# Kernel optimization log

Measured on AMD Instinct MI355X. Metric: run time of the kernel, lower is better.

The kernel has to match this reference:

```python
import jax, jax.numpy as jnp
import numpy as np

BN_EPS = 1e-5
K_HOPS = 10


def setup_inputs() -> dict:
    key = jax.random.key(0)
    ks = jax.random.split(key, 8)
    N, F, H, C, E = 169343, 128, 256, 40, 1200000
    return {
        "x": jax.random.normal(ks[0], (N, F), dtype=jnp.float32),
        "edge_index": jax.random.randint(ks[1], (2, E), 0, N, dtype=jnp.int64),
        "norm": jax.random.uniform(ks[2], (E,), dtype=jnp.float32),
        "W1": jax.random.normal(ks[3], (F, H), dtype=jnp.float32) * (1.0 / np.sqrt(F)),
        "b1": jnp.zeros((H,), jnp.float32),
        "bn_gamma": jnp.ones((H,), jnp.float32),
        "bn_beta": jnp.zeros((H,), jnp.float32),
        "bn_mean": jnp.zeros((H,), jnp.float32),
        "bn_var": jnp.ones((H,), jnp.float32),
        "W2": jax.random.normal(ks[4], (H, C), dtype=jnp.float32) * (1.0 / np.sqrt(H)),
        "b2": jnp.zeros((C,), jnp.float32),
        "proj_w": jax.random.normal(ks[5], (C,), dtype=jnp.float32) * (1.0 / np.sqrt(C)),
        "proj_b": jnp.zeros((1,), jnp.float32),
    }


def reference(x, edge_index, norm, W1, b1, bn_gamma, bn_beta, bn_mean, bn_var,
              W2, b2, proj_w, proj_b):
    N = x.shape[0]
    src, dst = edge_index[0], edge_index[1]

    # MLP head: Linear -> BatchNorm (eval, running stats) -> ReLU -> Linear
    h = x @ W1 + b1
    h = (h - bn_mean) * jax.lax.rsqrt(bn_var + BN_EPS) * bn_gamma + bn_beta
    h = jax.nn.relu(h)  # dropout: identity at inference
    h = h @ W2 + b2  # [N, C]

    # K-hop norm-weighted scatter-add propagation, collecting snapshots
    def hop(carry, _):
        msgs = norm[:, None] * carry[src]              # [E, C]
        nxt = jax.ops.segment_sum(msgs, dst, num_segments=N)
        return nxt, nxt

    _, hops = jax.lax.scan(hop, h, None, length=K_HOPS)  # [K, N, C]
    pps = jnp.concatenate([h[None], hops], axis=0)       # [K+1, N, C]
    pps = jnp.transpose(pps, (1, 0, 2))                  # [N, K+1, C]

    # sigmoid attention over hops, weighted combine
    retain = jax.nn.sigmoid(pps @ proj_w + proj_b[0])    # [N, K+1]
    out = jnp.einsum("nk,nkc->nc", retain, pps)          # [N, C]
    return jax.nn.log_softmax(out, axis=1)
```

## Files before the change

### kernel.cpp

```cpp
#include <hip/hip_runtime.h>
#include <hip/hip_bf16.h>
#include <math.h>

#define F 128
#define H 256
#define C 40
#define KHOPS 10
#define TM 64
#define HK 64

__global__ void k_count(const int* __restrict__ dst, int E, int* __restrict__ cnt) {
    int e = blockIdx.x * 256 + threadIdx.x;
    if (e < E) atomicAdd(&cnt[dst[e]], 1);
}

__global__ void k_scan1(const int* __restrict__ cnt, int n, int* __restrict__ bsum) {
    __shared__ int sh[256];
    int t = threadIdx.x;
    int base = blockIdx.x * 4096 + t * 16;
    int s = 0;
    for (int i = 0; i < 16; i++) { int idx = base + i; if (idx < n) s += cnt[idx]; }
    sh[t] = s; __syncthreads();
    for (int o = 128; o > 0; o >>= 1) {
        if (t < o) sh[t] += sh[t + o];
        __syncthreads();
    }
    if (t == 0) bsum[blockIdx.x] = sh[0];
}

__global__ void k_scan2(int* __restrict__ bsum, int nb) {
    if (threadIdx.x == 0) {
        int acc = 0;
        for (int i = 0; i < nb; i++) { int v = bsum[i]; bsum[i] = acc; acc += v; }
    }
}

__global__ void k_scan3(const int* __restrict__ cnt, int n, const int* __restrict__ bsum,
                        int* __restrict__ rp) {
    __shared__ int sh[256];
    int t = threadIdx.x;
    int base = blockIdx.x * 4096 + t * 16;
    int local[16]; int s = 0;
    for (int i = 0; i < 16; i++) {
        int idx = base + i;
        int v = (idx < n) ? cnt[idx] : 0;
        local[i] = v; s += v;
    }
    sh[t] = s; __syncthreads();
    for (int o = 1; o < 256; o <<= 1) {
        int v = (t >= o) ? sh[t - o] : 0;
        __syncthreads();
        sh[t] += v;
        __syncthreads();
    }
    int excl = (t == 0) ? 0 : sh[t - 1];
    int run = bsum[blockIdx.x] + excl;
    for (int i = 0; i < 16; i++) {
        int idx = base + i;
        if (idx < n) { rp[idx] = run; run += local[i]; }
    }
}

__global__ void k_fill(const int* __restrict__ src, const int* __restrict__ dst,
                       const float* __restrict__ nrm, int E, const int* __restrict__ rp,
                       int* __restrict__ cur, int2* __restrict__ ep) {
    int e = blockIdx.x * 256 + threadIdx.x;
    if (e < E) {
        int d = dst[e];
        int p = rp[d] + atomicAdd(&cur[d], 1);
        ep[p] = make_int2(src[e], __float_as_int(nrm[e]));
    }
}

__launch_bounds__(256, 2)
__global__ void k_mlp(const float* __restrict__ x, const float* __restrict__ W1,
                      const float* __restrict__ b1, const float* __restrict__ g,
                      const float* __restrict__ be, const float* __restrict__ mu,
                      const float* __restrict__ var, const float* __restrict__ W2,
                      const float* __restrict__ b2, const float* __restrict__ pw,
                      const float* __restrict__ pb,
                      float* __restrict__ h, float* __restrict__ oacc, int N) {
    __shared__ float xs[TM][132];
    __shared__ float h1s[TM][68];
    __shared__ float w2s[C][68];
    __shared__ float asc[HK], dsc[HK];
    __shared__ float redc[256];
    __shared__ float sigv[TM];

    int t = threadIdx.x;
    int n0 = blockIdx.x * TM;

    for (int k = 0; k < 8; k++) {
        int idx = k * 256 + t;
        int node = idx >> 5, f4 = idx & 31;
        int n = n0 + node;
        float4 v = (n < N) ? ((const float4*)x)[(size_t)n * (F / 4) + f4]
                           : make_float4(0.f, 0.f, 0.f, 0.f);
        *((float4*)&xs[node][f4 * 4]) = v;
    }

    float acc2[10];
    {
        int cg = t & 3;
        #pragma unroll
        for (int j = 0; j < 10; j++) acc2[j] = b2[cg * 10 + j];
    }

    int tn = t & 15, th = t >> 4;
    const float4* W1g = (const float4*)W1;

    for (int h0 = 0; h0 < H; h0 += HK) {
        for (int k = 0; k < 10; k++) {
            int idx = k * 256 + t;
            int hh = idx / 40, c = idx % 40;
            w2s[c][hh] = W2[(size_t)(h0 + hh) * C + c];
        }
        if (t < HK) {
            int hg = h0 + t;
            float a = g[hg] * rsqrtf(var[hg] + 1e-5f);
            asc[t] = a;
            dsc[t] = (b1[hg] - mu[hg]) * a + be[hg];
        }
        __syncthreads();

        float acc[4][4];
        #pragma unroll
        for (int i = 0; i < 4; i++)
            #pragma unroll
            for (int j = 0; j < 4; j++) acc[i][j] = 0.f;

        #pragma unroll 4
        for (int f0 = 0; f0 < F; f0 += 4) {
            float4 wv[4];
            #pragma unroll
            for (int q = 0; q < 4; q++)
                wv[q] = W1g[(size_t)(f0 + q) * (H / 4) + (h0 >> 2) + th];
            float4 xv[4];
            #pragma unroll
            for (int i = 0; i < 4; i++)
                xv[i] = *((const float4*)&xs[tn + 16 * i][f0]);
            #pragma unroll
            for (int i = 0; i < 4; i++) {
                float xa[4] = {xv[i].x, xv[i].y, xv[i].z, xv[i].w};
                #pragma unroll
                for (int q = 0; q < 4; q++) {
                    float wa[4] = {wv[q].x, wv[q].y, wv[q].z, wv[q].w};
                    #pragma unroll
                    for (int j = 0; j < 4; j++) acc[i][j] += xa[q] * wa[j];
                }
            }
        }
        #pragma unroll
        for (int i = 0; i < 4; i++) {
            float4 o;
            float* po = (float*)&o;
            #pragma unroll
            for (int j = 0; j < 4; j++) {
                int hh = th * 4 + j;
                float v = acc[i][j] * asc[hh] + dsc[hh];
                po[j] = v > 0.f ? v : 0.f;
            }
            *((float4*)&h1s[tn + 16 * i][th * 4]) = o;
        }
        __syncthreads();

        int n_loc = t >> 2, cg = t & 3;
        #pragma unroll 4
        for (int hh = 0; hh < HK; hh += 4) {
            float4 hv = *((const float4*)&h1s[n_loc][hh]);
            #pragma unroll
            for (int j = 0; j < 10; j++) {
                float4 w4 = *((const float4*)&w2s[cg * 10 + j][hh]);
                acc2[j] += hv.x * w4.x + hv.y * w4.y + hv.z * w4.z + hv.w * w4.w;
            }
        }
        __syncthreads();
    }

    int n_loc = t >> 2, cg = t & 3;
    int n = n0 + n_loc;
    float part = 0.f;
    #pragma unroll
    for (int j = 0; j < 10; j++) part += acc2[j] * pw[cg * 10 + j];
    redc[t] = part;
    __syncthreads();
    if (cg == 0) {
        float s = redc[n_loc * 4] + redc[n_loc * 4 + 1] + redc[n_loc * 4 + 2] + redc[n_loc * 4 + 3];
        sigv[n_loc] = 1.f / (1.f + expf(-(s + pb[0])));
    }
    __syncthreads();
    if (n < N) {
        float sg = sigv[n_loc];
        #pragma unroll
        for (int j = 0; j < 10; j++) {
            h[(size_t)n * C + cg * 10 + j] = acc2[j];
            oacc[(size_t)n * C + cg * 10 + j] = sg * acc2[j];
        }
    }
}

__global__ void k_hop(const float4* __restrict__ cur4, float4* __restrict__ nxt4,
                      float4* __restrict__ oacc4, const int* __restrict__ rp,
                      const int2* __restrict__ ep,
                      const float* __restrict__ pw, const float* __restrict__ pb, int N) {
    __shared__ float red[320];
    __shared__ float sig[64];
    int t = threadIdx.x;
    int nl = t / 5, p = t % 5;
    int n = blockIdx.x * 64 + nl;
    int c0 = 2 * p;
    float4 a0 = make_float4(0.f, 0.f, 0.f, 0.f);
    float4 a1 = make_float4(0.f, 0.f, 0.f, 0.f);
    if (n < N) {
        int b = rp[n], e = rp[n + 1];
        int j = b;
        for (; j + 4 <= e; j += 4) {
            int2 e0 = ep[j], e1 = ep[j + 1], e2 = ep[j + 2], e3 = ep[j + 3];
            const float4* r0 = cur4 + (size_t)e0.x * 10 + c0;
            const float4* r1 = cur4 + (size_t)e1.x * 10 + c0;
            const float4* r2 = cur4 + (size_t)e2.x * 10 + c0;
            const float4* r3 = cur4 + (size_t)e3.x * 10 + c0;
            float4 v00 = r0[0], v01 = r0[1];
            float4 v10 = r1[0], v11 = r1[1];
            float4 v20 = r2[0], v21 = r2[1];
            float4 v30 = r3[0], v31 = r3[1];
            float w0 = __int_as_float(e0.y), w1 = __int_as_float(e1.y);
            float w2 = __int_as_float(e2.y), w3 = __int_as_float(e3.y);
            a0.x += w0 * v00.x; a0.y += w0 * v00.y; a0.z += w0 * v00.z; a0.w += w0 * v00.w;
            a1.x += w0 * v01.x; a1.y += w0 * v01.y; a1.z += w0 * v01.z; a1.w += w0 * v01.w;
            a0.x += w1 * v10.x; a0.y += w1 * v10.y; a0.z += w1 * v10.z; a0.w += w1 * v10.w;
            a1.x += w1 * v11.x; a1.y += w1 * v11.y; a1.z += w1 * v11.z; a1.w += w1 * v11.w;
            a0.x += w2 * v20.x; a0.y += w2 * v20.y; a0.z += w2 * v20.z; a0.w += w2 * v20.w;
            a1.x += w2 * v21.x; a1.y += w2 * v21.y; a1.z += w2 * v21.z; a1.w += w2 * v21.w;
            a0.x += w3 * v30.x; a0.y += w3 * v30.y; a0.z += w3 * v30.z; a0.w += w3 * v30.w;
            a1.x += w3 * v31.x; a1.y += w3 * v31.y; a1.z += w3 * v31.z; a1.w += w3 * v31.w;
        }
        if (j + 2 <= e) {
            int2 e0 = ep[j], e1 = ep[j + 1];
            const float4* r0 = cur4 + (size_t)e0.x * 10 + c0;
            const float4* r1 = cur4 + (size_t)e1.x * 10 + c0;
            float4 v00 = r0[0], v01 = r0[1];
            float4 v10 = r1[0], v11 = r1[1];
            float w0 = __int_as_float(e0.y), w1 = __int_as_float(e1.y);
            a0.x += w0 * v00.x; a0.y += w0 * v00.y; a0.z += w0 * v00.z; a0.w += w0 * v00.w;
            a1.x += w0 * v01.x; a1.y += w0 * v01.y; a1.z += w0 * v01.z; a1.w += w0 * v01.w;
            a0.x += w1 * v10.x; a0.y += w1 * v10.y; a0.z += w1 * v10.z; a0.w += w1 * v10.w;
            a1.x += w1 * v11.x; a1.y += w1 * v11.y; a1.z += w1 * v11.z; a1.w += w1 * v11.w;
            j += 2;
        }
        if (j < e) {
            int2 e0 = ep[j];
            const float4* r0 = cur4 + (size_t)e0.x * 10 + c0;
            float4 v00 = r0[0], v01 = r0[1];
            float w0 = __int_as_float(e0.y);
            a0.x += w0 * v00.x; a0.y += w0 * v00.y; a0.z += w0 * v00.z; a0.w += w0 * v00.w;
            a1.x += w0 * v01.x; a1.y += w0 * v01.y; a1.z += w0 * v01.z; a1.w += w0 * v01.w;
        }
        nxt4[(size_t)n * 10 + c0] = a0;
        nxt4[(size_t)n * 10 + c0 + 1] = a1;
    }
    float4 pw0 = ((const float4*)pw)[c0];
    float4 pw1 = ((const float4*)pw)[c0 + 1];
    red[t] = a0.x * pw0.x + a0.y * pw0.y + a0.z * pw0.z + a0.w * pw0.w
           + a1.x * pw1.x + a1.y * pw1.y + a1.z * pw1.z + a1.w * pw1.w;
    __syncthreads();
    if (p == 0) {
        float s = red[t] + red[t + 1] + red[t + 2] + red[t + 3] + red[t + 4];
        sig[nl] = 1.f / (1.f + expf(-(s + pb[0])));
    }
    __syncthreads();
    if (n < N) {
        float sg = sig[nl];
        size_t o = (size_t)n * 10 + c0;
        float4 v0 = oacc4[o], v1 = oacc4[o + 1];
        v0.x += sg * a0.x; v0.y += sg * a0.y; v0.z += sg * a0.z; v0.w += sg * a0.w;
        v1.x += sg * a1.x; v1.y += sg * a1.y; v1.z += sg * a1.z; v1.w += sg * a1.w;
        oacc4[o] = v0;
        oacc4[o + 1] = v1;
    }
}

__global__ void k_lsm(float4* __restrict__ io, int N) {
    __shared__ float red[320];
    __shared__ float statm[32];
    __shared__ float stats[32];
    int t = threadIdx.x;
    int nl = t / 10, c4 = t % 10;
    int n = blockIdx.x * 32 + nl;
    bool ok = n < N;
    float4 v = ok ? io[(size_t)n * 10 + c4] : make_float4(-1e30f, -1e30f, -1e30f, -1e30f);
    red[t] = fmaxf(fmaxf(v.x, v.y), fmaxf(v.z, v.w));
    __syncthreads();
    if (c4 == 0) {
        float m = -1e30f;
        #pragma unroll
        for (int q = 0; q < 10; q++) m = fmaxf(m, red[nl * 10 + q]);
        statm[nl] = m;
    }
    __syncthreads();
    float m = statm[nl];
    float e0 = expf(v.x - m), e1 = expf(v.y - m), e2 = expf(v.z - m), e3 = expf(v.w - m);
    red[t] = e0 + e1 + e2 + e3;
    __syncthreads();
    if (c4 == 0) {
        float s = 0.f;
        #pragma unroll
        for (int q = 0; q < 10; q++) s += red[nl * 10 + q];
        stats[nl] = logf(s);
    }
    __syncthreads();
    if (ok) {
        float ls = stats[nl];
        io[(size_t)n * 10 + c4] = make_float4(v.x - m - ls, v.y - m - ls, v.z - m - ls, v.w - m - ls);
    }
}

extern "C" void kernel_launch(void* const* d_in, const int* in_sizes, int n_in,
                              void* d_out, int out_size, void* d_ws, size_t ws_size,
                              hipStream_t stream) {
    const float* x   = (const float*)d_in[0];
    const int*   ei  = (const int*)d_in[1];
    const float* nrm = (const float*)d_in[2];
    const float* W1  = (const float*)d_in[3];
    const float* b1  = (const float*)d_in[4];
    const float* g   = (const float*)d_in[5];
    const float* be  = (const float*)d_in[6];
    const float* mu  = (const float*)d_in[7];
    const float* var = (const float*)d_in[8];
    const float* W2  = (const float*)d_in[9];
    const float* b2  = (const float*)d_in[10];
    const float* pw  = (const float*)d_in[11];
    const float* pb  = (const float*)d_in[12];
    float* out = (float*)d_out;

    int N = in_sizes[0] / F;
    int E = in_sizes[2];

    char* w = (char*)d_ws;
    auto alloc = [&](size_t bytes) {
        void* p = (void*)w;
        w += ((bytes + 255) / 256) * 256;
        return p;
    };
    int*   rp     = (int*)alloc((size_t)(N + 1) * 4);
    int*   cursor = (int*)alloc((size_t)(N + 1) * 4);
    int*   bsum   = (int*)alloc(256 * 4);
    int2*  ep     = (int2*)alloc((size_t)E * 8);
    float* bufA   = (float*)alloc((size_t)N * C * 4);
    float* bufB   = (float*)alloc((size_t)N * C * 4);

    hipMemsetAsync(cursor, 0, (size_t)(N + 1) * 4, stream);

    k_count<<<(E + 255) / 256, 256, 0, stream>>>(ei + E, E, cursor);

    int n1 = N + 1;
    int NB = (n1 + 4095) / 4096;
    k_scan1<<<NB, 256, 0, stream>>>(cursor, n1, bsum);
    k_scan2<<<1, 64, 0, stream>>>(bsum, NB);
    k_scan3<<<NB, 256, 0, stream>>>(cursor, n1, bsum, rp);

    hipMemsetAsync(cursor, 0, (size_t)(N + 1) * 4, stream);
    k_fill<<<(E + 255) / 256, 256, 0, stream>>>(ei, ei + E, nrm, E, rp, cursor, ep);

    k_mlp<<<(N + TM - 1) / TM, 256, 0, stream>>>(x, W1, b1, g, be, mu, var, W2, b2,
                                                 pw, pb, bufA, out, N);

    int nodeBlocks64 = (N + 63) / 64;
    float* cur = bufA;
    float* nxt = bufB;
    for (int k = 0; k < KHOPS; k++) {
        k_hop<<<nodeBlocks64, 320, 0, stream>>>((const float4*)cur, (float4*)nxt, (float4*)out,
                                                rp, ep, pw, pb, N);
        float* tmp = cur; cur = nxt; nxt = tmp;
    }

    int nodeBlocks32 = (N + 31) / 32;
    k_lsm<<<nodeBlocks32, 320, 0, stream>>>((float4*)out, N);
}
```

Measured before the change: 1.136 ms.

## Pad hop feature rows to 64 floats and read transposed W2 from global

Hop feature buffers are padded to a 64-float row pitch, chosen only when the workspace is large enough, so that each gathered node row lines up with 256-byte boundaries during the scatter-gather hops. W2 is pre-transposed by a small kernel and the MLP reads it straight from global/L2 rather than staging it in shared memory each tile. Occupancy is raised to 3 blocks per CU, and outputs are written as coalesced float4 stores through LDS. The padding adds memory footprint and bandwidth on the writes, and the uncached W2 reads may add latency.

```diff
diff --git a/kernel.cpp b/kernel.cpp
--- a/kernel.cpp
+++ b/kernel.cpp
@@ -72,17 +72,21 @@
     }
 }
 
-__launch_bounds__(256, 2)
+__global__ void k_wt(const float* __restrict__ W2, float* __restrict__ w2t) {
+    int t = blockIdx.x * 256 + threadIdx.x;
+    if (t < H * C) { int h = t / C, c = t % C; w2t[c * H + h] = W2[t]; }
+}
+
+__launch_bounds__(256, 3)
 __global__ void k_mlp(const float* __restrict__ x, const float* __restrict__ W1,
                       const float* __restrict__ b1, const float* __restrict__ g,
                       const float* __restrict__ be, const float* __restrict__ mu,
-                      const float* __restrict__ var, const float* __restrict__ W2,
+                      const float* __restrict__ var, const float* __restrict__ w2t,
                       const float* __restrict__ b2, const float* __restrict__ pw,
                       const float* __restrict__ pb,
-                      float* __restrict__ h, float* __restrict__ oacc, int N) {
+                      float* __restrict__ hbuf, int cp, float* __restrict__ oacc, int N) {
     __shared__ float xs[TM][132];
     __shared__ float h1s[TM][68];
-    __shared__ float w2s[C][68];
     __shared__ float asc[HK], dsc[HK];
     __shared__ float redc[256];
     __shared__ float sigv[TM];
@@ -108,13 +112,9 @@
 
     int tn = t & 15, th = t >> 4;
     const float4* W1g = (const float4*)W1;
+    const float4* w2t4 = (const float4*)w2t;
 
     for (int h0 = 0; h0 < H; h0 += HK) {
-        for (int k = 0; k < 10; k++) {
-            int idx = k * 256 + t;
-            int hh = idx / 40, c = idx % 40;
-            w2s[c][hh] = W2[(size_t)(h0 + hh) * C + c];
-        }
         if (t < HK) {
             int hg = h0 + t;
             float a = g[hg] * rsqrtf(var[hg] + 1e-5f);
@@ -170,7 +170,7 @@
             float4 hv = *((const float4*)&h1s[n_loc][hh]);
             #pragma unroll
             for (int j = 0; j < 10; j++) {
-                float4 w4 = *((const float4*)&w2s[cg * 10 + j][hh]);
+                float4 w4 = w2t4[(size_t)(cg * 10 + j) * (H / 4) + ((h0 + hh) >> 2)];
                 acc2[j] += hv.x * w4.x + hv.y * w4.y + hv.z * w4.z + hv.w * w4.w;
             }
         }
@@ -178,7 +178,8 @@
     }
 
     int n_loc = t >> 2, cg = t & 3;
-    int n = n0 + n_loc;
+    #pragma unroll
+    for (int j = 0; j < 10; j++) h1s[n_loc][cg * 10 + j] = acc2[j];
     float part = 0.f;
     #pragma unroll
     for (int j = 0; j < 10; j++) part += acc2[j] * pw[cg * 10 + j];
@@ -189,19 +190,33 @@
         sigv[n_loc] = 1.f / (1.f + expf(-(s + pb[0])));
     }
     __syncthreads();
-    if (n < N) {
-        float sg = sigv[n_loc];
-        #pragma unroll
-        for (int j = 0; j < 10; j++) {
-            h[(size_t)n * C + cg * 10 + j] = acc2[j];
-            oacc[(size_t)n * C + cg * 10 + j] = sg * acc2[j];
+    for (int k = 0; k < 2; k++) {
+        int idx = k * 256 + t;
+        if (idx < 320) {
+            int row = idx / 5, p = idx % 5;
+            int n = n0 + row;
+            if (n < N) {
+                float4 a, b;
+                a.x = h1s[row][8 * p + 0]; a.y = h1s[row][8 * p + 1];
+                a.z = h1s[row][8 * p + 2]; a.w = h1s[row][8 * p + 3];
+                b.x = h1s[row][8 * p + 4]; b.y = h1s[row][8 * p + 5];
+                b.z = h1s[row][8 * p + 6]; b.w = h1s[row][8 * p + 7];
+                float4* hp = (float4*)(hbuf + (size_t)n * cp + 8 * p);
+                hp[0] = a; hp[1] = b;
+                float sg = sigv[row];
+                float4 oa, ob;
+                oa.x = sg * a.x; oa.y = sg * a.y; oa.z = sg * a.z; oa.w = sg * a.w;
+                ob.x = sg * b.x; ob.y = sg * b.y; ob.z = sg * b.z; ob.w = sg * b.w;
+                float4* op = (float4*)(oacc + (size_t)n * C + 8 * p);
+                op[0] = oa; op[1] = ob;
+            }
         }
     }
 }
 
 __global__ void k_hop(const float4* __restrict__ cur4, float4* __restrict__ nxt4,
                       float4* __restrict__ oacc4, const int* __restrict__ rp,
-                      const int2* __restrict__ ep,
+                      const int2* __restrict__ ep, int cp4,
                       const float* __restrict__ pw, const float* __restrict__ pb, int N) {
     __shared__ float red[320];
     __shared__ float sig[64];
@@ -216,10 +231,10 @@
         int j = b;
         for (; j + 4 <= e; j += 4) {
             int2 e0 = ep[j], e1 = ep[j + 1], e2 = ep[j + 2], e3 = ep[j + 3];
-            const float4* r0 = cur4 + (size_t)e0.x * 10 + c0;
-            const float4* r1 = cur4 + (size_t)e1.x * 10 + c0;
-            const float4* r2 = cur4 + (size_t)e2.x * 10 + c0;
-            const float4* r3 = cur4 + (size_t)e3.x * 10 + c0;
+            const float4* r0 = cur4 + (size_t)e0.x * cp4 + c0;
+            const float4* r1 = cur4 + (size_t)e1.x * cp4 + c0;
+            const float4* r2 = cur4 + (size_t)e2.x * cp4 + c0;
+            const float4* r3 = cur4 + (size_t)e3.x * cp4 + c0;
             float4 v00 = r0[0], v01 = r0[1];
             float4 v10 = r1[0], v11 = r1[1];
             float4 v20 = r2[0], v21 = r2[1];
@@ -237,8 +252,8 @@
         }
         if (j + 2 <= e) {
             int2 e0 = ep[j], e1 = ep[j + 1];
-            const float4* r0 = cur4 + (size_t)e0.x * 10 + c0;
-            const float4* r1 = cur4 + (size_t)e1.x * 10 + c0;
+            const float4* r0 = cur4 + (size_t)e0.x * cp4 + c0;
+            const float4* r1 = cur4 + (size_t)e1.x * cp4 + c0;
             float4 v00 = r0[0], v01 = r0[1];
             float4 v10 = r1[0], v11 = r1[1];
             float w0 = __int_as_float(e0.y), w1 = __int_as_float(e1.y);
@@ -250,14 +265,14 @@
         }
         if (j < e) {
             int2 e0 = ep[j];
-            const float4* r0 = cur4 + (size_t)e0.x * 10 + c0;
+            const float4* r0 = cur4 + (size_t)e0.x * cp4 + c0;
             float4 v00 = r0[0], v01 = r0[1];
             float w0 = __int_as_float(e0.y);
             a0.x += w0 * v00.x; a0.y += w0 * v00.y; a0.z += w0 * v00.z; a0.w += w0 * v00.w;
             a1.x += w0 * v01.x; a1.y += w0 * v01.y; a1.z += w0 * v01.z; a1.w += w0 * v01.w;
         }
-        nxt4[(size_t)n * 10 + c0] = a0;
-        nxt4[(size_t)n * 10 + c0 + 1] = a1;
+        nxt4[(size_t)n * cp4 + c0] = a0;
+        nxt4[(size_t)n * cp4 + c0 + 1] = a1;
     }
     float4 pw0 = ((const float4*)pw)[c0];
     float4 pw1 = ((const float4*)pw)[c0 + 1];
@@ -336,6 +351,11 @@
     int N = in_sizes[0] / F;
     int E = in_sizes[2];
 
+    auto alup = [](size_t b) { return ((b + 255) / 256) * 256; };
+    size_t fixedB = alup((size_t)(N + 1) * 4) * 2 + alup(1024) + alup((size_t)E * 8)
+                  + alup((size_t)H * C * 4);
+    int cp = (ws_size >= fixedB + 2 * alup((size_t)N * 64 * 4)) ? 64 : 40;
+
     char* w = (char*)d_ws;
     auto alloc = [&](size_t bytes) {
         void* p = (void*)w;
@@ -344,10 +364,11 @@
     };
     int*   rp     = (int*)alloc((size_t)(N + 1) * 4);
     int*   cursor = (int*)alloc((size_t)(N + 1) * 4);
-    int*   bsum   = (int*)alloc(256 * 4);
+    int*   bsum   = (int*)alloc(1024);
     int2*  ep     = (int2*)alloc((size_t)E * 8);
-    float* bufA   = (float*)alloc((size_t)N * C * 4);
-    float* bufB   = (float*)alloc((size_t)N * C * 4);
+    float* w2t    = (float*)alloc((size_t)H * C * 4);
+    float* bufA   = (float*)alloc((size_t)N * cp * 4);
+    float* bufB   = (float*)alloc((size_t)N * cp * 4);
 
     hipMemsetAsync(cursor, 0, (size_t)(N + 1) * 4, stream);
 
@@ -362,15 +383,17 @@
     hipMemsetAsync(cursor, 0, (size_t)(N + 1) * 4, stream);
     k_fill<<<(E + 255) / 256, 256, 0, stream>>>(ei, ei + E, nrm, E, rp, cursor, ep);
 
-    k_mlp<<<(N + TM - 1) / TM, 256, 0, stream>>>(x, W1, b1, g, be, mu, var, W2, b2,
-                                                 pw, pb, bufA, out, N);
+    k_wt<<<(H * C + 255) / 256, 256, 0, stream>>>(W2, w2t);
+
+    k_mlp<<<(N + TM - 1) / TM, 256, 0, stream>>>(x, W1, b1, g, be, mu, var, w2t, b2,
+                                                 pw, pb, bufA, cp, out, N);
 
     int nodeBlocks64 = (N + 63) / 64;
     float* cur = bufA;
     float* nxt = bufB;
     for (int k = 0; k < KHOPS; k++) {
         k_hop<<<nodeBlocks64, 320, 0, stream>>>((const float4*)cur, (float4*)nxt, (float4*)out,
-                                                rp, ep, pw, pb, N);
+                                                rp, ep, cp / 4, pw, pb, N);
         float* tmp = cur; cur = nxt; nxt = tmp;
     }
 
```

Result: slower. 1.829 ms (+61.0%).

## Halve MLP node tile, raise occupancy, and stage outputs for coalesced float4 stores

Applied to the files above, without the earlier changes.

Shrinks the MLP tile from 64 to 32 nodes per block and raises the launch bound to 4 blocks per CU. Each thread now owns half the first-layer accumulators and 5 instead of 10 output classes, which cuts register and LDS use so more waves can hide latency. The final h and weighted-output rows are staged through shared memory and written as contiguous float4 pairs rather than strided scalar stores. The cost is twice as many blocks, each reloading the W1 and W2 slices, so weight reuse per block drops.

```diff
diff --git a/kernel.cpp b/kernel.cpp
--- a/kernel.cpp
+++ b/kernel.cpp
@@ -6,7 +6,7 @@
 #define H 256
 #define C 40
 #define KHOPS 10
-#define TM 64
+#define TM 32
 #define HK 64
 
 __global__ void k_count(const int* __restrict__ dst, int E, int* __restrict__ cnt) {
@@ -72,14 +72,14 @@
     }
 }
 
-__launch_bounds__(256, 2)
+__launch_bounds__(256, 4)
 __global__ void k_mlp(const float* __restrict__ x, const float* __restrict__ W1,
                       const float* __restrict__ b1, const float* __restrict__ g,
                       const float* __restrict__ be, const float* __restrict__ mu,
                       const float* __restrict__ var, const float* __restrict__ W2,
                       const float* __restrict__ b2, const float* __restrict__ pw,
                       const float* __restrict__ pb,
-                      float* __restrict__ h, float* __restrict__ oacc, int N) {
+                      float* __restrict__ hbuf, float* __restrict__ oacc, int N) {
     __shared__ float xs[TM][132];
     __shared__ float h1s[TM][68];
     __shared__ float w2s[C][68];
@@ -90,7 +90,7 @@
     int t = threadIdx.x;
     int n0 = blockIdx.x * TM;
 
-    for (int k = 0; k < 8; k++) {
+    for (int k = 0; k < 4; k++) {
         int idx = k * 256 + t;
         int node = idx >> 5, f4 = idx & 31;
         int n = n0 + node;
@@ -99,12 +99,10 @@
         *((float4*)&xs[node][f4 * 4]) = v;
     }
 
-    float acc2[10];
-    {
-        int cg = t & 3;
-        #pragma unroll
-        for (int j = 0; j < 10; j++) acc2[j] = b2[cg * 10 + j];
-    }
+    int n_loc = t >> 3, cg = t & 7;
+    float acc2[5];
+    #pragma unroll
+    for (int j = 0; j < 5; j++) acc2[j] = b2[cg * 5 + j];
 
     int tn = t & 15, th = t >> 4;
     const float4* W1g = (const float4*)W1;
@@ -123,9 +121,9 @@
         }
         __syncthreads();
 
-        float acc[4][4];
-        #pragma unroll
-        for (int i = 0; i < 4; i++)
+        float acc[2][4];
+        #pragma unroll
+        for (int i = 0; i < 2; i++)
             #pragma unroll
             for (int j = 0; j < 4; j++) acc[i][j] = 0.f;
 
@@ -135,12 +133,12 @@
             #pragma unroll
             for (int q = 0; q < 4; q++)
                 wv[q] = W1g[(size_t)(f0 + q) * (H / 4) + (h0 >> 2) + th];
-            float4 xv[4];
-            #pragma unroll
-            for (int i = 0; i < 4; i++)
+            float4 xv[2];
+            #pragma unroll
+            for (int i = 0; i < 2; i++)
                 xv[i] = *((const float4*)&xs[tn + 16 * i][f0]);
             #pragma unroll
-            for (int i = 0; i < 4; i++) {
+            for (int i = 0; i < 2; i++) {
                 float xa[4] = {xv[i].x, xv[i].y, xv[i].z, xv[i].w};
                 #pragma unroll
                 for (int q = 0; q < 4; q++) {
@@ -151,7 +149,7 @@
             }
         }
         #pragma unroll
-        for (int i = 0; i < 4; i++) {
+        for (int i = 0; i < 2; i++) {
             float4 o;
             float* po = (float*)&o;
             #pragma unroll
@@ -164,37 +162,49 @@
         }
         __syncthreads();
 
-        int n_loc = t >> 2, cg = t & 3;
         #pragma unroll 4
         for (int hh = 0; hh < HK; hh += 4) {
             float4 hv = *((const float4*)&h1s[n_loc][hh]);
             #pragma unroll
-            for (int j = 0; j < 10; j++) {
-                float4 w4 = *((const float4*)&w2s[cg * 10 + j][hh]);
+            for (int j = 0; j < 5; j++) {
+                float4 w4 = *((const float4*)&w2s[cg * 5 + j][hh]);
                 acc2[j] += hv.x * w4.x + hv.y * w4.y + hv.z * w4.z + hv.w * w4.w;
             }
         }
         __syncthreads();
     }
 
-    int n_loc = t >> 2, cg = t & 3;
-    int n = n0 + n_loc;
+    #pragma unroll
+    for (int j = 0; j < 5; j++) h1s[n_loc][cg * 5 + j] = acc2[j];
     float part = 0.f;
     #pragma unroll
-    for (int j = 0; j < 10; j++) part += acc2[j] * pw[cg * 10 + j];
+    for (int j = 0; j < 5; j++) part += acc2[j] * pw[cg * 5 + j];
     redc[t] = part;
     __syncthreads();
     if (cg == 0) {
-        float s = redc[n_loc * 4] + redc[n_loc * 4 + 1] + redc[n_loc * 4 + 2] + redc[n_loc * 4 + 3];
+        float s = 0.f;
+        #pragma unroll
+        for (int q = 0; q < 8; q++) s += redc[n_loc * 8 + q];
         sigv[n_loc] = 1.f / (1.f + expf(-(s + pb[0])));
     }
     __syncthreads();
-    if (n < N) {
-        float sg = sigv[n_loc];
-        #pragma unroll
-        for (int j = 0; j < 10; j++) {
-            h[(size_t)n * C + cg * 10 + j] = acc2[j];
-            oacc[(size_t)n * C + cg * 10 + j] = sg * acc2[j];
+    if (t < 160) {
+        int row = t / 5, p = t % 5;
+        int n = n0 + row;
+        if (n < N) {
+            float4 a, b;
+            a.x = h1s[row][8 * p + 0]; a.y = h1s[row][8 * p + 1];
+            a.z = h1s[row][8 * p + 2]; a.w = h1s[row][8 * p + 3];
+            b.x = h1s[row][8 * p + 4]; b.y = h1s[row][8 * p + 5];
+            b.z = h1s[row][8 * p + 6]; b.w = h1s[row][8 * p + 7];
+            float4* hp = (float4*)(hbuf + (size_t)n * C + 8 * p);
+            hp[0] = a; hp[1] = b;
+            float sg = sigv[row];
+            float4 oa, ob;
+            oa.x = sg * a.x; oa.y = sg * a.y; oa.z = sg * a.z; oa.w = sg * a.w;
+            ob.x = sg * b.x; ob.y = sg * b.y; ob.z = sg * b.z; ob.w = sg * b.w;
+            float4* op = (float4*)(oacc + (size_t)n * C + 8 * p);
+            op[0] = oa; op[1] = ob;
         }
     }
 }
@@ -344,7 +354,7 @@
     };
     int*   rp     = (int*)alloc((size_t)(N + 1) * 4);
     int*   cursor = (int*)alloc((size_t)(N + 1) * 4);
-    int*   bsum   = (int*)alloc(256 * 4);
+    int*   bsum   = (int*)alloc(1024);
     int2*  ep     = (int2*)alloc((size_t)E * 8);
     float* bufA   = (float*)alloc((size_t)N * C * 4);
     float* bufB   = (float*)alloc((size_t)N * C * 4);
```

Measured after the change: 1.199 ms. 5.5% more time.
